# Kernel tuning notes

Hardware: AMD Instinct MI355X
Metric: run time of the kernel (lower is better)

The kernel has to match this reference:

```python
import jax, jax.numpy as jnp
import numpy as np

N_NODES = 100_000
N_EDGES = 1_600_000
N_GRAPHS = 64
IN_CH = 128
HID = 64
OUT_CH = 2


def setup_inputs() -> dict:
    key = jax.random.key(0)
    ks = jax.random.split(key, 12)

    def lin(k, fan_in, fan_out):
        s = 1.0 / np.sqrt(fan_in)
        return jax.random.uniform(k, (fan_in, fan_out), jnp.float32, -s, s)

    x = jax.random.normal(ks[0], (N_NODES, IN_CH), jnp.float32)
    edge_index = jax.random.randint(ks[1], (2, N_EDGES), 0, N_NODES, jnp.int64)
    batch = jnp.sort(jax.random.randint(ks[2], (N_NODES,), 0, N_GRAPHS, jnp.int64))
    return {
        "x": x,
        "edge_index": edge_index,
        "batch": batch,
        "w_rel0": lin(ks[3], IN_CH, HID),
        "b_rel0": jnp.zeros((HID,), jnp.float32),
        "w_root0": lin(ks[4], IN_CH, HID),
        "w_rel1": lin(ks[5], HID, HID),
        "b_rel1": jnp.zeros((HID,), jnp.float32),
        "w_root1": lin(ks[6], HID, HID),
        "w_rel2": lin(ks[7], HID, HID),
        "b_rel2": jnp.zeros((HID,), jnp.float32),
        "w_root2": lin(ks[8], HID, HID),
        "head_w1": lin(ks[9], HID, HID),
        "head_b1": jnp.zeros((HID,), jnp.float32),
        "head_w2": lin(ks[10], HID, OUT_CH),
        "head_b2": jnp.zeros((OUT_CH,), jnp.float32),
    }


def _graph_conv(x, src, dst, w_rel, b_rel, w_root):
    # PyG GraphConv: out = lin_rel(sum_{j->i} x_j) + lin_root(x_i)
    agg = jax.ops.segment_sum(x[src], dst, num_segments=N_NODES)  # [N, d_in]
    return agg @ w_rel + b_rel + x @ w_root


def reference(x, edge_index, batch, w_rel0, b_rel0, w_root0,
              w_rel1, b_rel1, w_root1, w_rel2, b_rel2, w_root2,
              head_w1, head_b1, head_w2, head_b2):
    src, dst = edge_index[0], edge_index[1]
    h = jax.nn.relu(_graph_conv(x, src, dst, w_rel0, b_rel0, w_root0))
    h = jax.nn.relu(_graph_conv(h, src, dst, w_rel1, b_rel1, w_root1))
    h = jax.nn.relu(_graph_conv(h, src, dst, w_rel2, b_rel2, w_root2))
    # global_mean_pool over graph ids (dropout is identity at inference)
    sums = jax.ops.segment_sum(h, batch, num_segments=N_GRAPHS)          # [G, H]
    cnts = jax.ops.segment_sum(jnp.ones((N_NODES,), h.dtype), batch,
                               num_segments=N_GRAPHS)                    # [G]
    pooled = sums / jnp.maximum(cnts, 1.0)[:, None]
    z = jax.nn.relu(pooled @ head_w1 + head_b1)
    return z @ head_w2 + head_b2
```

## Files before the change

kernel.cpp:

```cpp
#include <hip/hip_runtime.h>
#include <hip/hip_bf16.h>

#define CAP 64
#define KBUCK 391
#define BSHIFT 8
#define BCAP 4608
#define CHUNK_A 2048
#define AITER (CHUNK_A / 256)
#define LDSZ 36864

typedef __attribute__((ext_vector_type(8))) short short8;
typedef __attribute__((ext_vector_type(4))) float f32x4;

__device__ inline unsigned short bfbits(float f) {
    __hip_bfloat16 b = __float2bfloat16(f);
    unsigned short u;
    __builtin_memcpy(&u, &b, 2);
    return u;
}

__device__ inline void bucket_body(char* smem, int bb, const int* __restrict__ ei,
                                   int E, int* __restrict__ gcur,
                                   unsigned* __restrict__ bucketed)
{
    int* hist = (int*)smem;
    int* base = hist + KBUCK;
    const int e0 = bb * CHUNK_A;
    const int e1 = min(e0 + CHUNK_A, E);
    for (int i = threadIdx.x; i < KBUCK; i += 256) hist[i] = 0;
    __syncthreads();
    int dreg[AITER];
    #pragma unroll
    for (int it = 0; it < AITER; ++it) {
        int e = e0 + it * 256 + threadIdx.x;
        dreg[it] = (e < e1) ? ei[E + e] : -1;
        if (dreg[it] >= 0) atomicAdd(&hist[dreg[it] >> BSHIFT], 1);
    }
    __syncthreads();
    for (int i = threadIdx.x; i < KBUCK; i += 256) {
        int h = hist[i];
        base[i] = h ? atomicAdd(&gcur[i], h) : 0;
        hist[i] = 0;
    }
    __syncthreads();
    #pragma unroll
    for (int it = 0; it < AITER; ++it) {
        int e = e0 + it * 256 + threadIdx.x;
        if (e < e1) {
            int s = ei[e];
            int d = dreg[it];
            int b = d >> BSHIFT;
            int off = base[b] + atomicAdd(&hist[b], 1);
            if (off < BCAP)
                bucketed[(size_t)b * BCAP + off] = ((unsigned)s << 8) | (unsigned)(d & 255);
        }
    }
}

__global__ __launch_bounds__(256) void build_slots_kernel(
    const unsigned* __restrict__ bucketed, const int* __restrict__ gcur,
    int* __restrict__ cnt, int* __restrict__ slots, int N)
{
    __shared__ int lcnt[256];
    const int b = blockIdx.x;
    const int nb0 = b << BSHIFT;
    lcnt[threadIdx.x] = 0;
    __syncthreads();
    const int count = min(gcur[b], BCAP);
    const unsigned* src = bucketed + (size_t)b * BCAP;
    for (int i = threadIdx.x; i < count; i += 256) {
        unsigned p = src[i];
        int dl = (int)(p & 255u);
        int pos = atomicAdd(&lcnt[dl], 1);
        if (pos < CAP) slots[(size_t)(nb0 + dl) * CAP + pos] = (int)(p >> 8);
    }
    __syncthreads();
    int node = nb0 + threadIdx.x;
    if (node < N) cnt[node] = min(lcnt[threadIdx.x], CAP);
}

__global__ __launch_bounds__(256) void prep_weights_kernel(
    const float* __restrict__ wr0, const float* __restrict__ wt0,
    const float* __restrict__ wr1, const float* __restrict__ wt1,
    const float* __restrict__ wr2, const float* __restrict__ wt2,
    __hip_bfloat16* __restrict__ hi, __hip_bfloat16* __restrict__ lo)
{
    int idx = blockIdx.x * 256 + threadIdx.x;
    if (idx >= 32768) return;
    const float *wr, *wt;
    int n, k;
    if (idx < 16384)      { wr = wr0; wt = wt0; int r = idx;         n = r >> 7; k = r & 127; }
    else if (idx < 24576) { wr = wr1; wt = wt1; int r = idx - 16384; n = r >> 6; k = r & 63; }
    else                  { wr = wr2; wt = wt2; int r = idx - 24576; n = r >> 6; k = r & 63; }
    float w = (n < 64) ? wr[k * 64 + n] : wt[k * 64 + (n - 64)];
    __hip_bfloat16 h = __float2bfloat16(w);
    hi[idx] = h;
    lo[idx] = __float2bfloat16(w - __bfloat162float(h));
}

template <int DIN, bool AFP32>
__device__ inline void mfma_body(
    char* smem, int bx, const void* __restrict__ featv,
    const __hip_bfloat16* __restrict__ whiT, const __hip_bfloat16* __restrict__ wloT,
    const float* __restrict__ b_rel,
    __hip_bfloat16* __restrict__ y, __hip_bfloat16* __restrict__ r, int N)
{
    __hip_bfloat16* As = (__hip_bfloat16*)smem;
    __hip_bfloat16* Bh = As + 128 * 48;
    __hip_bfloat16* Bl = Bh + 128 * 48;
    const int t = threadIdx.x;
    const int lane = t & 63;
    const int wid = t >> 6;
    const int wm = wid >> 1, wn = wid & 1;
    const int node0 = bx * 128;
    const int lrow = lane & 15;
    const int kgrp = lane >> 4;

    f32x4 acc[4][4];
    #pragma unroll
    for (int i = 0; i < 4; ++i)
        #pragma unroll
        for (int j = 0; j < 4; ++j) acc[i][j] = (f32x4){0.f, 0.f, 0.f, 0.f};

    for (int ks = 0; ks < DIN / 32; ++ks) {
        #pragma unroll
        for (int p = 0; p < 2; ++p) {
            int c = t + p * 256;
            int m = c >> 2, kc = c & 3;
            int row = node0 + m; if (row >= N) row = N - 1;
            if (AFP32) {
                const float* feat = (const float*)featv;
                const float* src = feat + (size_t)row * DIN + ks * 32 + kc * 8;
                float4 v0 = *(const float4*)src;
                float4 v1 = *(const float4*)(src + 4);
                union { uint4 q; unsigned short s[8]; } pk;
                pk.s[0] = bfbits(v0.x); pk.s[1] = bfbits(v0.y);
                pk.s[2] = bfbits(v0.z); pk.s[3] = bfbits(v0.w);
                pk.s[4] = bfbits(v1.x); pk.s[5] = bfbits(v1.y);
                pk.s[6] = bfbits(v1.z); pk.s[7] = bfbits(v1.w);
                *(uint4*)&As[m * 48 + kc * 8] = pk.q;
            } else {
                const __hip_bfloat16* feat = (const __hip_bfloat16*)featv;
                *(uint4*)&As[m * 48 + kc * 8] =
                    *(const uint4*)(feat + (size_t)row * DIN + ks * 32 + kc * 8);
            }
        }
        #pragma unroll
        for (int p = 0; p < 4; ++p) {
            int c = t + p * 256;
            int half = c >> 9;
            int cc = c & 511;
            int n = cc >> 2, kc = cc & 3;
            const __hip_bfloat16* w = half ? wloT : whiT;
            uint4 v = *(const uint4*)(w + (size_t)n * DIN + ks * 32 + kc * 8);
            if (half) *(uint4*)&Bl[n * 48 + kc * 8] = v;
            else      *(uint4*)&Bh[n * 48 + kc * 8] = v;
        }
        __syncthreads();

        short8 a[4], bh[4], bl[4];
        #pragma unroll
        for (int i = 0; i < 4; ++i)
            a[i] = *(const short8*)&As[(wm * 64 + i * 16 + lrow) * 48 + kgrp * 8];
        #pragma unroll
        for (int j = 0; j < 4; ++j) {
            bh[j] = *(const short8*)&Bh[(wn * 64 + j * 16 + lrow) * 48 + kgrp * 8];
            bl[j] = *(const short8*)&Bl[(wn * 64 + j * 16 + lrow) * 48 + kgrp * 8];
        }
        #pragma unroll
        for (int i = 0; i < 4; ++i)
            #pragma unroll
            for (int j = 0; j < 4; ++j) {
                acc[i][j] = __builtin_amdgcn_mfma_f32_16x16x32_bf16(a[i], bh[j], acc[i][j], 0, 0, 0);
                acc[i][j] = __builtin_amdgcn_mfma_f32_16x16x32_bf16(a[i], bl[j], acc[i][j], 0, 0, 0);
            }
        __syncthreads();
    }

    #pragma unroll
    for (int i = 0; i < 4; ++i) {
        int mbase = node0 + wm * 64 + i * 16 + kgrp * 4;
        #pragma unroll
        for (int j = 0; j < 4; ++j) {
            int n = wn * 64 + j * 16 + lrow;
            #pragma unroll
            for (int v = 0; v < 4; ++v) {
                int m = mbase + v;
                if (m < N) {
                    float val = acc[i][j][v];
                    if (n < 64) y[(size_t)m * 64 + n] = __float2bfloat16(val);
                    else        r[(size_t)m * 64 + (n - 64)] = __float2bfloat16(val + b_rel[n - 64]);
                }
            }
        }
    }
}

__global__ __launch_bounds__(256) void fused_l0_kernel(
    const float* __restrict__ x,
    const __hip_bfloat16* __restrict__ whiT, const __hip_bfloat16* __restrict__ wloT,
    const float* __restrict__ b_rel,
    __hip_bfloat16* __restrict__ y, __hip_bfloat16* __restrict__ r, int N,
    int gemm_blocks, const int* __restrict__ ei, int E,
    int* __restrict__ gcur, unsigned* __restrict__ bucketed)
{
    extern __shared__ char smem[];
    if ((int)blockIdx.x < gemm_blocks)
        mfma_body<128, true>(smem, blockIdx.x, x, whiT, wloT, b_rel, y, r, N);
    else
        bucket_body(smem, blockIdx.x - gemm_blocks, ei, E, gcur, bucketed);
}

template <int DIN>
__global__ __launch_bounds__(256) void mfma_lin_kernel(
    const __hip_bfloat16* __restrict__ feat,
    const __hip_bfloat16* __restrict__ whiT, const __hip_bfloat16* __restrict__ wloT,
    const float* __restrict__ b_rel,
    __hip_bfloat16* __restrict__ y, __hip_bfloat16* __restrict__ r, int N)
{
    extern __shared__ char smem[];
    mfma_body<DIN, false>(smem, blockIdx.x, feat, whiT, wloT, b_rel, y, r, N);
}

__global__ __launch_bounds__(256) void gather_relu_kernel(
    const __hip_bfloat16* __restrict__ y, const int* __restrict__ cnt,
    const int* __restrict__ slots, const __hip_bfloat16* __restrict__ rin,
    __hip_bfloat16* __restrict__ hout, int N)
{
    const int node = blockIdx.x * 8 + (threadIdx.x >> 5);
    if (node >= N) return;
    const int sub = threadIdx.x & 31;
    const int nb = sub >> 3;
    const int ch = (sub & 7) * 8;
    const int deg = cnt[node];
    const int* sl = slots + (size_t)node * CAP;
    const unsigned short* yp = (const unsigned short*)y;

    float a[8], b[8];
    #pragma unroll
    for (int k = 0; k < 8; ++k) { a[k] = 0.f; b[k] = 0.f; }

    #pragma unroll 2
    for (int j = nb; j < deg; j += 8) {
        int n0 = sl[j];
        uint4 v = *(const uint4*)(yp + (size_t)n0 * 64 + ch);
        a[0] += __uint_as_float(v.x << 16); a[1] += __uint_as_float(v.x & 0xffff0000u);
        a[2] += __uint_as_float(v.y << 16); a[3] += __uint_as_float(v.y & 0xffff0000u);
        a[4] += __uint_as_float(v.z << 16); a[5] += __uint_as_float(v.z & 0xffff0000u);
        a[6] += __uint_as_float(v.w << 16); a[7] += __uint_as_float(v.w & 0xffff0000u);
        int j2 = j + 4;
        if (j2 < deg) {
            int n1 = sl[j2];
            uint4 w = *(const uint4*)(yp + (size_t)n1 * 64 + ch);
            b[0] += __uint_as_float(w.x << 16); b[1] += __uint_as_float(w.x & 0xffff0000u);
            b[2] += __uint_as_float(w.y << 16); b[3] += __uint_as_float(w.y & 0xffff0000u);
            b[4] += __uint_as_float(w.z << 16); b[5] += __uint_as_float(w.z & 0xffff0000u);
            b[6] += __uint_as_float(w.w << 16); b[7] += __uint_as_float(w.w & 0xffff0000u);
        }
    }
    #pragma unroll
    for (int k = 0; k < 8; ++k) {
        a[k] += b[k];
        a[k] += __shfl_xor(a[k], 8);
        a[k] += __shfl_xor(a[k], 16);
    }
    if (nb == 0) {
        uint4 rv = *(const uint4*)((const unsigned short*)rin + (size_t)node * 64 + ch);
        float r0 = __uint_as_float(rv.x << 16), r1 = __uint_as_float(rv.x & 0xffff0000u);
        float r2 = __uint_as_float(rv.y << 16), r3 = __uint_as_float(rv.y & 0xffff0000u);
        float r4 = __uint_as_float(rv.z << 16), r5 = __uint_as_float(rv.z & 0xffff0000u);
        float r6 = __uint_as_float(rv.w << 16), r7 = __uint_as_float(rv.w & 0xffff0000u);
        float f0 = fmaxf(r0 + a[0], 0.f), f1 = fmaxf(r1 + a[1], 0.f);
        float f2 = fmaxf(r2 + a[2], 0.f), f3 = fmaxf(r3 + a[3], 0.f);
        float f4 = fmaxf(r4 + a[4], 0.f), f5 = fmaxf(r5 + a[5], 0.f);
        float f6 = fmaxf(r6 + a[6], 0.f), f7 = fmaxf(r7 + a[7], 0.f);
        union { uint4 q; unsigned short s[8]; } pk;
        pk.s[0] = bfbits(f0); pk.s[1] = bfbits(f1); pk.s[2] = bfbits(f2); pk.s[3] = bfbits(f3);
        pk.s[4] = bfbits(f4); pk.s[5] = bfbits(f5); pk.s[6] = bfbits(f6); pk.s[7] = bfbits(f7);
        *(uint4*)((unsigned short*)hout + (size_t)node * 64 + ch) = pk.q;
    }
}

__global__ __launch_bounds__(256) void pool_kernel(
    const __hip_bfloat16* __restrict__ h, const int* __restrict__ batch,
    float* __restrict__ gsum, int* __restrict__ gcnt, int N)
{
    const int CHUNK = 64;
    int wid = (blockIdx.x * 256 + threadIdx.x) >> 6;
    int lane = threadIdx.x & 63;
    int nb = lane >> 3;
    int ch = (lane & 7) * 8;
    int start = wid * CHUNK;
    if (start >= N) return;
    int end = min(start + CHUNK, N);
    const unsigned short* hp = (const unsigned short*)h;

    float a[8];
    #pragma unroll
    for (int k = 0; k < 8; ++k) a[k] = 0.f;
    int runcnt = 0;
    int i = start;
    int gcur = batch[start];

    while (i < end) {
        int idx = i + lane; if (idx > end - 1) idx = end - 1;
        int bl = batch[idx];
        unsigned long long diff = __ballot(bl != gcur && (i + lane) < end);
        int len = diff ? ((int)__ffsll(diff) - 1) : min(64, end - i);
        for (int j = i + nb; j < i + len; j += 8) {
            uint4 v = *(const uint4*)(hp + (size_t)j * 64 + ch);
            a[0] += __uint_as_float(v.x << 16); a[1] += __uint_as_float(v.x & 0xffff0000u);
            a[2] += __uint_as_float(v.y << 16); a[3] += __uint_as_float(v.y & 0xffff0000u);
            a[4] += __uint_as_float(v.z << 16); a[5] += __uint_as_float(v.z & 0xffff0000u);
            a[6] += __uint_as_float(v.w << 16); a[7] += __uint_as_float(v.w & 0xffff0000u);
        }
        runcnt += len;
        i += len;
        if (diff) {
            #pragma unroll
            for (int k = 0; k < 8; ++k) {
                a[k] += __shfl_xor(a[k], 8);
                a[k] += __shfl_xor(a[k], 16);
                a[k] += __shfl_xor(a[k], 32);
            }
            if (runcnt > 0) {
                if (nb == 0) {
                    #pragma unroll
                    for (int k = 0; k < 8; ++k)
                        atomicAdd(&gsum[gcur * 64 + ch + k], a[k]);
                }
                if (lane == 0) atomicAdd(&gcnt[gcur], runcnt);
            }
            #pragma unroll
            for (int k = 0; k < 8; ++k) a[k] = 0.f;
            runcnt = 0;
            gcur = __shfl(bl, len);
        }
    }
    #pragma unroll
    for (int k = 0; k < 8; ++k) {
        a[k] += __shfl_xor(a[k], 8);
        a[k] += __shfl_xor(a[k], 16);
        a[k] += __shfl_xor(a[k], 32);
    }
    if (runcnt > 0) {
        if (nb == 0) {
            #pragma unroll
            for (int k = 0; k < 8; ++k)
                atomicAdd(&gsum[gcur * 64 + ch + k], a[k]);
        }
        if (lane == 0) atomicAdd(&gcnt[gcur], runcnt);
    }
}

__global__ __launch_bounds__(256) void head_kernel(
    const float* __restrict__ gsum, const int* __restrict__ gcnt,
    const float* __restrict__ w1, const float* __restrict__ b1,
    const float* __restrict__ w2, const float* __restrict__ b2,
    float* __restrict__ out)
{
    __shared__ float pm[64 * 64];
    __shared__ float z[64 * 64];
    int t = threadIdx.x;
    for (int i = t; i < 64 * 64; i += 256) {
        int g = i >> 6;
        float cf = (float)gcnt[g];
        if (cf < 1.f) cf = 1.f;
        pm[i] = gsum[i] / cf;
    }
    __syncthreads();
    for (int i = t; i < 64 * 64; i += 256) {
        int g = i >> 6, c = i & 63;
        float a = b1[c];
        #pragma unroll 8
        for (int k = 0; k < 64; ++k) a = fmaf(pm[g * 64 + k], w1[k * 64 + c], a);
        z[i] = fmaxf(a, 0.f);
    }
    __syncthreads();
    for (int i = t; i < 64 * 2; i += 256) {
        int g = i >> 1, o = i & 1;
        float a = b2[o];
        #pragma unroll 8
        for (int k = 0; k < 64; ++k) a = fmaf(z[g * 64 + k], w2[k * 2 + o], a);
        out[i] = a;
    }
}

extern "C" void kernel_launch(void* const* d_in, const int* in_sizes, int n_in,
                              void* d_out, int out_size, void* d_ws, size_t ws_size,
                              hipStream_t stream)
{
    const float* x       = (const float*)d_in[0];
    const int*   ei      = (const int*)d_in[1];
    const int*   batch   = (const int*)d_in[2];
    const float* w_rel0  = (const float*)d_in[3];
    const float* b_rel0  = (const float*)d_in[4];
    const float* w_root0 = (const float*)d_in[5];
    const float* w_rel1  = (const float*)d_in[6];
    const float* b_rel1  = (const float*)d_in[7];
    const float* w_root1 = (const float*)d_in[8];
    const float* w_rel2  = (const float*)d_in[9];
    const float* b_rel2  = (const float*)d_in[10];
    const float* w_root2 = (const float*)d_in[11];
    const float* hw1     = (const float*)d_in[12];
    const float* hb1     = (const float*)d_in[13];
    const float* hw2     = (const float*)d_in[14];
    const float* hb2     = (const float*)d_in[15];
    float* out = (float*)d_out;

    const int N = in_sizes[0] / 128;
    const int E = in_sizes[1] / 2;
    const int G = 64;

    size_t off = 0;
    auto alloc = [&](size_t bytes) -> void* {
        void* p = (char*)d_ws + off;
        off += (bytes + 255) & ~(size_t)255;
        return p;
    };
    int*      cnt      = (int*)alloc((size_t)N * 4);
    int*      slots    = (int*)alloc((size_t)N * CAP * 4);
    unsigned* bucketed = (unsigned*)alloc((size_t)KBUCK * BCAP * 4);
    int*      gcur     = (int*)alloc((size_t)KBUCK * 4);
    __hip_bfloat16* whiT = (__hip_bfloat16*)alloc(32768 * 2);
    __hip_bfloat16* wloT = (__hip_bfloat16*)alloc(32768 * 2);
    __hip_bfloat16* ybf  = (__hip_bfloat16*)alloc((size_t)N * 64 * 2);
    __hip_bfloat16* h0   = (__hip_bfloat16*)alloc((size_t)N * 64 * 2);
    __hip_bfloat16* h1   = (__hip_bfloat16*)alloc((size_t)N * 64 * 2);
    __hip_bfloat16* rbf  = (__hip_bfloat16*)alloc((size_t)N * 64 * 2);
    float* gsum     = (float*)alloc((size_t)G * 64 * 4);
    int*   gcnt     = (int*)alloc((size_t)G * 4);
    (void)ws_size; (void)n_in;

    hipMemsetAsync(gcur, 0, (size_t)KBUCK * 4, stream);
    hipMemsetAsync(gsum, 0, (size_t)G * 64 * 4, stream);
    hipMemsetAsync(gcnt, 0, (size_t)G * 4, stream);

    prep_weights_kernel<<<128, 256, 0, stream>>>(w_rel0, w_root0, w_rel1, w_root1,
                                                 w_rel2, w_root2, whiT, wloT);

    const int gemm_blocks = (N + 127) / 128;
    const int bucket_blocks = (E + CHUNK_A - 1) / CHUNK_A;
    const int gather_blocks = (N + 7) / 8;

    fused_l0_kernel<<<gemm_blocks + bucket_blocks, 256, LDSZ, stream>>>(
        x, whiT, wloT, b_rel0, ybf, rbf, N, gemm_blocks, ei, E, gcur, bucketed);
    build_slots_kernel<<<KBUCK, 256, 0, stream>>>(bucketed, gcur, cnt, slots, N);
    gather_relu_kernel<<<gather_blocks, 256, 0, stream>>>(ybf, cnt, slots, rbf, h0, N);

    mfma_lin_kernel<64><<<gemm_blocks, 256, LDSZ, stream>>>(
        h0, whiT + 16384, wloT + 16384, b_rel1, ybf, rbf, N);
    gather_relu_kernel<<<gather_blocks, 256, 0, stream>>>(ybf, cnt, slots, rbf, h1, N);

    mfma_lin_kernel<64><<<gemm_blocks, 256, LDSZ, stream>>>(
        h1, whiT + 24576, wloT + 24576, b_rel2, ybf, rbf, N);
    gather_relu_kernel<<<gather_blocks, 256, 0, stream>>>(ybf, cnt, slots, rbf, h0, N);

    int pool_waves  = (N + 63) / 64;
    int pool_blocks = (pool_waves + 3) / 4;
    pool_kernel<<<pool_blocks, 256, 0, stream>>>(h0, batch, gsum, gcnt, N);
    head_kernel<<<1, 256, 0, stream>>>(gsum, gcnt, hw1, hb1, hw2, hb2, out);
}
```

Baseline: 374.5 us.

## Pad bucket counters, fold memsets into prep kernel, drop LDS in layer GEMMs

Bucket cursors are padded to one per 64-byte stride, so the global atomics from many blocks no longer contend on shared cache lines. The three memset calls are removed and the zeroing moves into the weight-prep kernel, which cuts launch overhead. The 64-input GEMM kernel now loads A and B fragments straight from global memory into MFMA registers with no LDS staging, which frees LDS and raises occupancy. The risk is uncoalesced scattered bf16 output stores and repeated global reads of the weights.

New measurement: 380.4 us. About the same (+1.6%).

```diff
diff --git a/kernel.cpp b/kernel.cpp
--- a/kernel.cpp
+++ b/kernel.cpp
@@ -7,6 +7,7 @@
 #define BCAP 4608
 #define CHUNK_A 2048
 #define AITER (CHUNK_A / 256)
+#define GPAD 16
 #define LDSZ 36864
 
 typedef __attribute__((ext_vector_type(8))) short short8;
@@ -39,7 +40,7 @@
     __syncthreads();
     for (int i = threadIdx.x; i < KBUCK; i += 256) {
         int h = hist[i];
-        base[i] = h ? atomicAdd(&gcur[i], h) : 0;
+        base[i] = h ? atomicAdd(&gcur[i * GPAD], h) : 0;
         hist[i] = 0;
     }
     __syncthreads();
@@ -66,7 +67,7 @@
     const int nb0 = b << BSHIFT;
     lcnt[threadIdx.x] = 0;
     __syncthreads();
-    const int count = min(gcur[b], BCAP);
+    const int count = min(gcur[b * GPAD], BCAP);
     const unsigned* src = bucketed + (size_t)b * BCAP;
     for (int i = threadIdx.x; i < count; i += 256) {
         unsigned p = src[i];
@@ -83,9 +84,13 @@
     const float* __restrict__ wr0, const float* __restrict__ wt0,
     const float* __restrict__ wr1, const float* __restrict__ wt1,
     const float* __restrict__ wr2, const float* __restrict__ wt2,
-    __hip_bfloat16* __restrict__ hi, __hip_bfloat16* __restrict__ lo)
+    __hip_bfloat16* __restrict__ hi, __hip_bfloat16* __restrict__ lo,
+    int* __restrict__ gcur, float* __restrict__ gsum, int* __restrict__ gcnt)
 {
     int idx = blockIdx.x * 256 + threadIdx.x;
+    if (idx < KBUCK * GPAD) gcur[idx] = 0;
+    if (idx < 64 * 64) gsum[idx] = 0.f;
+    if (idx < 64) gcnt[idx] = 0;
     if (idx >= 32768) return;
     const float *wr, *wt;
     int n, k;
@@ -218,8 +223,61 @@
     const float* __restrict__ b_rel,
     __hip_bfloat16* __restrict__ y, __hip_bfloat16* __restrict__ r, int N)
 {
-    extern __shared__ char smem[];
-    mfma_body<DIN, false>(smem, blockIdx.x, feat, whiT, wloT, b_rel, y, r, N);
+    const int t = threadIdx.x;
+    const int lane = t & 63;
+    const int wid = t >> 6;
+    const int wm = wid >> 1, wn = wid & 1;
+    const int node0 = blockIdx.x * 128;
+    const int lrow = lane & 15;
+    const int kgrp = lane >> 4;
+
+    f32x4 acc[4][4];
+    #pragma unroll
+    for (int i = 0; i < 4; ++i)
+        #pragma unroll
+        for (int j = 0; j < 4; ++j) acc[i][j] = (f32x4){0.f, 0.f, 0.f, 0.f};
+
+    #pragma unroll
+    for (int ks = 0; ks < DIN / 32; ++ks) {
+        short8 a[4], bh[4], bl[4];
+        #pragma unroll
+        for (int i = 0; i < 4; ++i) {
+            int row = node0 + wm * 64 + i * 16 + lrow;
+            if (row >= N) row = N - 1;
+            a[i] = *(const short8*)(feat + (size_t)row * DIN + ks * 32 + kgrp * 8);
+        }
+        #pragma unroll
+        for (int j = 0; j < 4; ++j) {
+            int n = wn * 64 + j * 16 + lrow;
+            bh[j] = *(const short8*)(whiT + (size_t)n * DIN + ks * 32 + kgrp * 8);
+            bl[j] = *(const short8*)(wloT + (size_t)n * DIN + ks * 32 + kgrp * 8);
+        }
+        #pragma unroll
+        for (int i = 0; i < 4; ++i)
+            #pragma unroll
+            for (int j = 0; j < 4; ++j) {
+                acc[i][j] = __builtin_amdgcn_mfma_f32_16x16x32_bf16(a[i], bh[j], acc[i][j], 0, 0, 0);
+                acc[i][j] = __builtin_amdgcn_mfma_f32_16x16x32_bf16(a[i], bl[j], acc[i][j], 0, 0, 0);
+            }
+    }
+
+    #pragma unroll
+    for (int i = 0; i < 4; ++i) {
+        int mbase = node0 + wm * 64 + i * 16 + kgrp * 4;
+        #pragma unroll
+        for (int j = 0; j < 4; ++j) {
+            int n = wn * 64 + j * 16 + lrow;
+            #pragma unroll
+            for (int v = 0; v < 4; ++v) {
+                int m = mbase + v;
+                if (m < N) {
+                    float val = acc[i][j][v];
+                    if (n < 64) y[(size_t)m * 64 + n] = __float2bfloat16(val);
+                    else        r[(size_t)m * 64 + (n - 64)] = __float2bfloat16(val + b_rel[n - 64]);
+                }
+            }
+        }
+    }
 }
 
 __global__ __launch_bounds__(256) void gather_relu_kernel(
@@ -421,7 +479,7 @@
     int*      cnt      = (int*)alloc((size_t)N * 4);
     int*      slots    = (int*)alloc((size_t)N * CAP * 4);
     unsigned* bucketed = (unsigned*)alloc((size_t)KBUCK * BCAP * 4);
-    int*      gcur     = (int*)alloc((size_t)KBUCK * 4);
+    int*      gcur     = (int*)alloc((size_t)KBUCK * GPAD * 4);
     __hip_bfloat16* whiT = (__hip_bfloat16*)alloc(32768 * 2);
     __hip_bfloat16* wloT = (__hip_bfloat16*)alloc(32768 * 2);
     __hip_bfloat16* ybf  = (__hip_bfloat16*)alloc((size_t)N * 64 * 2);
@@ -432,12 +490,9 @@
     int*   gcnt     = (int*)alloc((size_t)G * 4);
     (void)ws_size; (void)n_in;
 
-    hipMemsetAsync(gcur, 0, (size_t)KBUCK * 4, stream);
-    hipMemsetAsync(gsum, 0, (size_t)G * 64 * 4, stream);
-    hipMemsetAsync(gcnt, 0, (size_t)G * 4, stream);
-
     prep_weights_kernel<<<128, 256, 0, stream>>>(w_rel0, w_root0, w_rel1, w_root1,
-                                                 w_rel2, w_root2, whiT, wloT);
+                                                 w_rel2, w_root2, whiT, wloT,
+                                                 gcur, gsum, gcnt);
 
     const int gemm_blocks = (N + 127) / 128;
     const int bucket_blocks = (E + CHUNK_A - 1) / CHUNK_A;
@@ -448,11 +503,11 @@
     build_slots_kernel<<<KBUCK, 256, 0, stream>>>(bucketed, gcur, cnt, slots, N);
     gather_relu_kernel<<<gather_blocks, 256, 0, stream>>>(ybf, cnt, slots, rbf, h0, N);
 
-    mfma_lin_kernel<64><<<gemm_blocks, 256, LDSZ, stream>>>(
+    mfma_lin_kernel<64><<<gemm_blocks, 256, 0, stream>>>(
         h0, whiT + 16384, wloT + 16384, b_rel1, ybf, rbf, N);
     gather_relu_kernel<<<gather_blocks, 256, 0, stream>>>(ybf, cnt, slots, rbf, h1, N);
 
-    mfma_lin_kernel<64><<<gemm_blocks, 256, LDSZ, stream>>>(
+    mfma_lin_kernel<64><<<gemm_blocks, 256, 0, stream>>>(
         h1, whiT + 24576, wloT + 24576, b_rel2, ybf, rbf, N);
     gather_relu_kernel<<<gather_blocks, 256, 0, stream>>>(ybf, cnt, slots, rbf, h0, N);
 
```
